# Optimization experiments

Hardware: AMD Instinct MI355X
Metric: run time of the kernel (lower is better)

The kernel has to match this reference:

```python
import jax, jax.numpy as jnp
import numpy as np

N_NODES = 50000
N_EDGES = 800000
NUM_RELATIONS = 8   # 2 * n_speakers**2 with n_speakers = 2
NUM_BASES = 30
G_DIM, H1_DIM, H2_DIM = 128, 128, 128


def setup_inputs() -> dict:
    key = jax.random.key(0)
    ks = jax.random.split(key, 10)
    inp = {
        "node_features": jax.random.normal(ks[0], (N_NODES, G_DIM), jnp.float32),
        "edge_index": jax.random.randint(ks[1], (2, N_EDGES), 0, N_NODES, dtype=jnp.int64),
        "edge_type": jax.random.randint(ks[2], (N_EDGES,), 0, NUM_RELATIONS, dtype=jnp.int64),
        "edge_norm": jax.random.uniform(ks[3], (N_EDGES,), jnp.float32),
        # RGCNConv params (basis decomposition)
        "basis": jax.random.normal(ks[4], (NUM_BASES, G_DIM, H1_DIM), jnp.float32) * 0.05,
        "comp": jax.random.normal(ks[5], (NUM_RELATIONS, NUM_BASES), jnp.float32) * 0.1,
        "root": jax.random.normal(ks[6], (G_DIM, H1_DIM), jnp.float32) * 0.05,
        "bias1": jnp.zeros((H1_DIM,), jnp.float32),
        # GraphConv params: lin_rel (with bias) applied to aggregated neighbors, lin_root (no bias)
        "w_rel": jax.random.normal(ks[7], (H1_DIM, H2_DIM), jnp.float32) * 0.05,
        "b_rel": jnp.zeros((H2_DIM,), jnp.float32),
        "w_root": jax.random.normal(ks[8], (H1_DIM, H2_DIM), jnp.float32) * 0.05,
    }
    return inp


def reference(node_features, edge_index, edge_type, edge_norm,
              basis, comp, root, bias1, w_rel, b_rel, w_root):
    src, dst = edge_index[0], edge_index[1]  # source_to_target flow (PyG default)

    # ---- Layer 1: RGCNConv with basis decomposition ----
    # W[r] = sum_b comp[r,b] * basis[b]  -> [R, g, h1]
    W = jnp.einsum('rb,bio->rio', comp, basis)
    # Project every node under every relation once (N*R*h1), then gather per edge.
    # Mathematically identical to per-edge x_j @ W[edge_type] but avoids an [E, g, h1] tensor.
    x_proj = jnp.einsum('ni,rio->nro', node_features, W)  # [N, R, h1]
    msg = x_proj[src, edge_type] * edge_norm[:, None]     # [E, h1]
    agg = jax.ops.segment_sum(msg, dst, num_segments=N_NODES)  # scatter-add to targets
    h = agg + node_features @ root + bias1                # [N, h1]

    # ---- Layer 2: GraphConv (aggr='add', no edge_weight) ----
    agg2 = jax.ops.segment_sum(h[src], dst, num_segments=N_NODES)  # [N, h1]
    out = agg2 @ w_rel + b_rel + h @ w_root               # [N, h2]
    return out
```

## Files before the change

kernel.cpp:

```cpp
#include <hip/hip_runtime.h>
#include <hip/hip_bf16.h>
#include <stdint.h>

#define N_NODES 50000
#define N_EDGES 800000
#define NREL    8
#define NBASES  30
#define DIM     128
#define NSLOT   9
#define NCAT    (NSLOT*DIM)
#define SCAN_NB ((N_NODES + 255) / 256)
#define NB_C    196
#define EPB_PLACE 2048
#define NBLK_PLACE ((N_EDGES + EPB_PLACE - 1) / EPB_PLACE)
#define M_T1    32
#define T1_BLOCKS ((N_NODES + M_T1 - 1) / M_T1)
#define APAD    1160
#define PREP_TOTAL  (NCAT * DIM + 2 * DIM * DIM)
#define PREP_BLKS   ((PREP_TOTAL + 255) / 256)
#define CONV_BLKS   ((N_NODES * DIM / 4 + 255) / 256)
#define HIST_BLKS   ((N_EDGES + 255) / 256)

typedef __attribute__((ext_vector_type(8))) short short8;
typedef __attribute__((ext_vector_type(4))) float floatx4;
typedef __hip_bfloat16  bf16;
typedef __hip_bfloat162 bf16x2;

__device__ inline ushort f2bu(float f) { bf16 b = __float2bfloat16(f); return *(ushort*)&b; }
__device__ inline float  bu2f(ushort u) { union { unsigned i; float f; } c; c.i = ((unsigned)u) << 16; return c.f; }

__global__ __launch_bounds__(256) void setup_kernel(const float* __restrict__ basis, const float* __restrict__ comp,
                                                    const float* __restrict__ root, const float* __restrict__ w_rel,
                                                    const float* __restrict__ w_root,
                                                    bf16* __restrict__ W2T, bf16* __restrict__ wrelT,
                                                    bf16* __restrict__ wrootT,
                                                    const float4* __restrict__ x4, ushort4* __restrict__ xb4,
                                                    const int* __restrict__ ei, int* __restrict__ deg) {
    int b = blockIdx.x;
    if (b < PREP_BLKS) {
        int idx = b * 256 + threadIdx.x;
        const int n_cat = NCAT * DIM;
        const int n_sq  = DIM * DIM;
        if (idx < n_cat) {
            int o = idx / NCAT;
            int rem = idx - o * NCAT;
            int r = rem >> 7, k = rem & 127;
            float v;
            if (r < NREL) {
                v = 0.f;
                for (int bb = 0; bb < NBASES; ++bb)
                    v += comp[r * NBASES + bb] * basis[(bb * DIM + k) * DIM + o];
            } else {
                v = root[k * DIM + o];
            }
            W2T[idx] = __float2bfloat16(v);
        } else if (idx < n_cat + n_sq) {
            int t = idx - n_cat; int k = t & 127, o = t >> 7;
            wrelT[o * DIM + k] = __float2bfloat16(w_rel[k * DIM + o]);
        } else if (idx < n_cat + 2 * n_sq) {
            int t = idx - n_cat - n_sq; int k = t & 127, o = t >> 7;
            wrootT[o * DIM + k] = __float2bfloat16(w_root[k * DIM + o]);
        }
    } else if (b < PREP_BLKS + CONV_BLKS) {
        int i = (b - PREP_BLKS) * 256 + threadIdx.x;
        int n4 = N_NODES * DIM / 4;
        if (i < n4) {
            float4 f = x4[i];
            ushort4 o;
            o.x = f2bu(f.x); o.y = f2bu(f.y); o.z = f2bu(f.z); o.w = f2bu(f.w);
            xb4[i] = o;
        }
    } else {
        int e = (b - PREP_BLKS - CONV_BLKS) * 256 + threadIdx.x;
        if (e < N_EDGES) atomicAdd(&deg[ei[N_EDGES + e]], 1);
    }
}

__global__ __launch_bounds__(256) void scan_one(const int* __restrict__ deg, int* __restrict__ segoff,
                                                unsigned long long* __restrict__ bstate, int n) {
    __shared__ int buf[256];
    int b = blockIdx.x, tid = threadIdx.x;
    int i = b * 256 + tid;
    int v = (i < n) ? deg[i] : 0;
    buf[tid] = v;
    __syncthreads();
#pragma unroll
    for (int o = 1; o < 256; o <<= 1) {
        int t = (tid >= o) ? buf[tid - o] : 0;
        __syncthreads();
        buf[tid] += t;
        __syncthreads();
    }
    int incl = buf[tid];
    int total = buf[255];
    if (tid == 0)
        __hip_atomic_store(&bstate[b], (1ULL << 32) | (unsigned)total,
                           __ATOMIC_RELEASE, __HIP_MEMORY_SCOPE_AGENT);
    int mysum = 0;
    for (int j = tid; j < b; j += 256) {
        unsigned long long s;
        do {
            s = __hip_atomic_load(&bstate[j], __ATOMIC_ACQUIRE, __HIP_MEMORY_SCOPE_AGENT);
        } while (!(s >> 32));
        mysum += (int)(s & 0xFFFFFFFFu);
    }
    __syncthreads();
    buf[tid] = mysum;
    __syncthreads();
#pragma unroll
    for (int o = 128; o > 0; o >>= 1) {
        if (tid < o) buf[tid] += buf[tid + o];
        __syncthreads();
    }
    int base = buf[0];
    if (i < n) segoff[i + 1] = base + incl;
    if (b == 0 && tid == 0) segoff[0] = 0;
}

__global__ __launch_bounds__(256) void place_kernel(const int* __restrict__ ei, const int* __restrict__ et,
                                                    const float* __restrict__ en, const int* __restrict__ segoff,
                                                    int* __restrict__ bcur, uint2* __restrict__ tmp) {
    __shared__ int lhist[NB_C];
    __shared__ int lbase[NB_C];
    __shared__ int lrank[NB_C];
    int tid = threadIdx.x;
    for (int i = tid; i < NB_C; i += 256) { lhist[i] = 0; lrank[i] = 0; }
    __syncthreads();
    int e0 = blockIdx.x * EPB_PLACE;
#pragma unroll
    for (int i = 0; i < EPB_PLACE / 256; ++i) {
        int e = e0 + i * 256 + tid;
        if (e < N_EDGES) atomicAdd(&lhist[ei[N_EDGES + e] >> 8], 1);
    }
    __syncthreads();
    for (int c = tid; c < NB_C; c += 256)
        if (lhist[c] > 0) lbase[c] = atomicAdd(&bcur[c], lhist[c]);
    __syncthreads();
#pragma unroll
    for (int i = 0; i < EPB_PLACE / 256; ++i) {
        int e = e0 + i * 256 + tid;
        if (e < N_EDGES) {
            int d = ei[N_EDGES + e];
            int c = d >> 8;
            int r = atomicAdd(&lrank[c], 1);
            int p = segoff[c << 8] + lbase[c] + r;
            tmp[p] = make_uint2((unsigned)ei[e] | ((unsigned)et[e] << 16) | ((unsigned)(d & 255) << 19),
                                __float_as_uint(en[e]));
        }
    }
}

__global__ __launch_bounds__(256) void sortb_kernel(const uint2* __restrict__ tmp, const int* __restrict__ segoff,
                                                    uint2* __restrict__ rec, int* __restrict__ typeoff) {
    __shared__ int hist2[256 * 8];
    int c = blockIdx.x;
    int tid = threadIdx.x;
    for (int i = tid; i < 256 * 8; i += 256) hist2[i] = 0;
    __syncthreads();
    int base = segoff[c << 8];
    int nlimit = (c + 1) << 8; if (nlimit > N_NODES) nlimit = N_NODES;
    int end = segoff[nlimit];
    for (int i = base + tid; i < end; i += 256) {
        unsigned x = tmp[i].x;
        int dl = (x >> 19) & 255, ty = (x >> 16) & 7;
        atomicAdd(&hist2[dl * 8 + ty], 1);
    }
    __syncthreads();
    {
        int node = (c << 8) + tid;
        if (node < N_NODES) {
            int run = segoff[node] - base;
            int offs[8];
#pragma unroll
            for (int t = 0; t < 8; ++t) {
                int cnt = hist2[tid * 8 + t];
                hist2[tid * 8 + t] = run;
                offs[t] = base + run;
                run += cnt;
            }
            *(int4*)(typeoff + (size_t)node * 8)     = make_int4(offs[0], offs[1], offs[2], offs[3]);
            *(int4*)(typeoff + (size_t)node * 8 + 4) = make_int4(offs[4], offs[5], offs[6], offs[7]);
        }
    }
    __syncthreads();
    for (int i = base + tid; i < end; i += 256) {
        uint2 r = tmp[i];
        int dl = (r.x >> 19) & 255, ty = (r.x >> 16) & 7;
        int p = base + atomicAdd(&hist2[dl * 8 + ty], 1);
        rec[p] = make_uint2(r.x & 0x7FFFFu, r.y);
    }
}

__device__ inline void flush8(ushort* dst, const float* acc) {
    short8 o;
#pragma unroll
    for (int f = 0; f < 8; ++f) o[f] = (short)f2bu(acc[f]);
    *(short8*)dst = o;
}

__global__ __launch_bounds__(512, 4) void rgcn1_kernel(const uint2* __restrict__ rec, const int* __restrict__ typeoff,
                                                       const int* __restrict__ segoff, const ushort* __restrict__ xb,
                                                       const ushort* __restrict__ W2Tu, const float* __restrict__ bias1,
                                                       ushort* __restrict__ H) {
    __shared__ ushort As[M_T1][APAD];
    int tm = blockIdx.x * M_T1;
    int tid = threadIdx.x;
    int quad = tid >> 4, kl = tid & 15;
    int node = tm + quad;

    int offs[10];
    if (node < N_NODES) {
        int4 o0 = *(const int4*)(typeoff + (size_t)node * 8);
        int4 o1 = *(const int4*)(typeoff + (size_t)node * 8 + 4);
        offs[0] = o0.x; offs[1] = o0.y; offs[2] = o0.z; offs[3] = o0.w;
        offs[4] = o1.x; offs[5] = o1.y; offs[6] = o1.z; offs[7] = o1.w;
        offs[8] = segoff[node + 1];
    } else {
#pragma unroll
        for (int t = 0; t < 9; ++t) offs[t] = 0;
    }
#pragma unroll
    for (int t = 0; t < 8; ++t) {
        float a8[8] = {0.f, 0.f, 0.f, 0.f, 0.f, 0.f, 0.f, 0.f};
        for (int eo = offs[t]; eo < offs[t + 1]; eo += 4) {
            int m = offs[t + 1] - eo; if (m > 4) m = 4;
            uint2 rr[4]; short8 vv[4];
#pragma unroll
            for (int j = 0; j < 4; ++j) if (j < m) rr[j] = rec[eo + j];
#pragma unroll
            for (int j = 0; j < 4; ++j) if (j < m)
                vv[j] = *(const short8*)(xb + (size_t)(rr[j].x & 0xFFFFu) * 128 + kl * 8);
#pragma unroll
            for (int j = 0; j < 4; ++j) if (j < m) {
                float nrm = __uint_as_float(rr[j].y);
#pragma unroll
                for (int f = 0; f < 8; ++f) a8[f] += nrm * bu2f((ushort)vv[j][f]);
            }
        }
        flush8(&As[quad][t * 128 + kl * 8], a8);
    }
    {
        short8 v = {0, 0, 0, 0, 0, 0, 0, 0};
        if (node < N_NODES) v = *(const short8*)(xb + (size_t)node * 128 + kl * 8);
        *(short8*)(&As[quad][8 * 128 + kl * 8]) = v;
    }
    __syncthreads();

    int wave = tid >> 6, lane = tid & 63;
    int q = lane >> 4, mr = lane & 15;
    floatx4 zero = {0.f, 0.f, 0.f, 0.f};
    floatx4 acc[2] = {zero, zero};
    const ushort* brow = W2Tu + (size_t)(wave * 16 + mr) * NCAT + q * 8;
    for (int kt = 0; kt < 36; ++kt) {
        short8 b  = *(const short8*)(brow + kt * 32);
        short8 a0 = *(const short8*)(&As[mr][kt * 32 + q * 8]);
        short8 a1 = *(const short8*)(&As[16 + mr][kt * 32 + q * 8]);
        acc[0] = __builtin_amdgcn_mfma_f32_16x16x32_bf16(a0, b, acc[0], 0, 0, 0);
        acc[1] = __builtin_amdgcn_mfma_f32_16x16x32_bf16(a1, b, acc[1], 0, 0, 0);
    }
    float bi = bias1[wave * 16 + mr];
#pragma unroll
    for (int rt = 0; rt < 2; ++rt)
#pragma unroll
        for (int r4 = 0; r4 < 4; ++r4) {
            int row = tm + rt * 16 + q * 4 + r4;
            if (row < N_NODES) H[(size_t)row * 128 + wave * 16 + mr] = f2bu(acc[rt][r4] + bi);
        }
}

__global__ void seg2_kernel(const uint2* __restrict__ rec, const int* __restrict__ segoff,
                            const ushort* __restrict__ h, ushort* __restrict__ out2) {
    int quad = threadIdx.x >> 4;
    int node = blockIdx.x * 16 + quad;
    if (node >= N_NODES) return;
    int lane = threadIdx.x & 15;
    int st = segoff[node], en = segoff[node + 1];
    float acc[8] = {0.f, 0.f, 0.f, 0.f, 0.f, 0.f, 0.f, 0.f};
    for (int chunk = st; chunk < en; chunk += 4) {
        int m = en - chunk; if (m > 4) m = 4;
        uint2 rr[4]; short8 vv[4];
#pragma unroll
        for (int j = 0; j < 4; ++j) if (j < m) rr[j] = rec[chunk + j];
#pragma unroll
        for (int j = 0; j < 4; ++j) if (j < m)
            vv[j] = *(const short8*)(h + (size_t)(rr[j].x & 0xFFFFu) * 128 + lane * 8);
#pragma unroll
        for (int j = 0; j < 4; ++j) if (j < m)
#pragma unroll
            for (int f = 0; f < 8; ++f) acc[f] += bu2f((ushort)vv[j][f]);
    }
    short8 o;
#pragma unroll
    for (int f = 0; f < 8; ++f) o[f] = (short)f2bu(acc[f]);
    *(short8*)(out2 + (size_t)node * 128 + lane * 8) = o;
}

__global__ __launch_bounds__(256) void gemm2_kernel(const bf16* __restrict__ A1, const bf16* __restrict__ B1T,
                                                    const bf16* __restrict__ A2, const bf16* __restrict__ B2T,
                                                    const float* __restrict__ brel, float* __restrict__ out, int M) {
    __shared__ ushort As[64][136];
    __shared__ ushort Bs[64][136];
    int tm = blockIdx.x * 64, tn = blockIdx.y * 64;
    int wave = threadIdx.x >> 6, lane = threadIdx.x & 63;
    int q = lane >> 4, mr = lane & 15;
    floatx4 zero = {0.f, 0.f, 0.f, 0.f};
    floatx4 acc[4] = {zero, zero, zero, zero};

    for (int phase = 0; phase < 2; ++phase) {
        const ushort* Au = (const ushort*)(phase ? A2 : A1);
        const ushort* Bu = (const ushort*)(phase ? B2T : B1T);
        if (phase) __syncthreads();
        for (int c = threadIdx.x; c < 64 * 16; c += 256) {
            int row = c >> 4, seg = c & 15;
            int gr = tm + row;
            short8 av = {0, 0, 0, 0, 0, 0, 0, 0};
            if (gr < M) av = *(const short8*)(Au + (size_t)gr * 128 + seg * 8);
            *(short8*)(&As[row][seg * 8]) = av;
            short8 bv = *(const short8*)(Bu + (size_t)(tn + row) * 128 + seg * 8);
            *(short8*)(&Bs[row][seg * 8]) = bv;
        }
        __syncthreads();
#pragma unroll
        for (int kt = 0; kt < 4; ++kt) {
            short8 a = *(const short8*)(&As[wave * 16 + mr][q * 8 + kt * 32]);
#pragma unroll
            for (int nt = 0; nt < 4; ++nt) {
                short8 b = *(const short8*)(&Bs[nt * 16 + mr][q * 8 + kt * 32]);
                acc[nt] = __builtin_amdgcn_mfma_f32_16x16x32_bf16(a, b, acc[nt], 0, 0, 0);
            }
        }
    }
    __syncthreads();
    float* Csf = (float*)&As[0][0];
#pragma unroll
    for (int nt = 0; nt < 4; ++nt)
#pragma unroll
        for (int r4 = 0; r4 < 4; ++r4) {
            int row = wave * 16 + q * 4 + r4;
            int col = nt * 16 + mr;
            Csf[row * 68 + col] = acc[nt][r4] + brel[tn + col];
        }
    __syncthreads();
#pragma unroll
    for (int u = 0; u < 4; ++u) {
        int cc = threadIdx.x + u * 256;
        int row = cc >> 4, seg = cc & 15;
        int gr = tm + row;
        if (gr < M) {
            float4 v = *(const float4*)(&Csf[row * 68 + seg * 4]);
            *(float4*)(out + (size_t)gr * 128 + tn + seg * 4) = v;
        }
    }
}

extern "C" void kernel_launch(void* const* d_in, const int* in_sizes, int n_in,
                              void* d_out, int out_size, void* d_ws, size_t ws_size,
                              hipStream_t stream) {
    const float* x      = (const float*)d_in[0];
    const int*   ei     = (const int*)d_in[1];
    const int*   et     = (const int*)d_in[2];
    const float* en     = (const float*)d_in[3];
    const float* basis  = (const float*)d_in[4];
    const float* comp   = (const float*)d_in[5];
    const float* root   = (const float*)d_in[6];
    const float* bias1  = (const float*)d_in[7];
    const float* w_rel  = (const float*)d_in[8];
    const float* b_rel  = (const float*)d_in[9];
    const float* w_root = (const float*)d_in[10];
    float* out = (float*)d_out;

    char* ws = (char*)d_ws;
    size_t off = 0;
    auto alloc = [&](size_t bytes) { size_t o = off; off += (bytes + 255) & ~(size_t)255; return o; };

    size_t o_deg    = alloc((size_t)N_NODES * 4);
    size_t o_bcur   = alloc((size_t)NB_C * 4);
    size_t o_bstate = alloc((size_t)SCAN_NB * 8);
    size_t o_segoff = alloc((size_t)(N_NODES + 1) * 4);
    size_t o_toff   = alloc((size_t)N_NODES * 8 * 4);
    size_t o_rec    = alloc((size_t)N_EDGES * 8);
    size_t o_tmp    = alloc((size_t)N_EDGES * 8);
    size_t o_w2t    = alloc((size_t)NCAT * DIM * 2);
    size_t o_wrel   = alloc((size_t)DIM * DIM * 2);
    size_t o_wroot  = alloc((size_t)DIM * DIM * 2);
    size_t o_xb     = alloc((size_t)N_NODES * DIM * 2);
    size_t o_hb     = alloc((size_t)N_NODES * DIM * 2);
    size_t o_agg2   = alloc((size_t)N_NODES * DIM * 2);

    int*   deg    = (int*)(ws + o_deg);
    int*   bcur   = (int*)(ws + o_bcur);
    unsigned long long* bstate = (unsigned long long*)(ws + o_bstate);
    int*   segoff = (int*)(ws + o_segoff);
    int*   toff   = (int*)(ws + o_toff);
    uint2* rec    = (uint2*)(ws + o_rec);
    uint2* tmp    = (uint2*)(ws + o_tmp);
    bf16*  w2t    = (bf16*)(ws + o_w2t);
    bf16*  wrelT  = (bf16*)(ws + o_wrel);
    bf16*  wrootT = (bf16*)(ws + o_wroot);
    bf16*  xb     = (bf16*)(ws + o_xb);
    bf16*  hb     = (bf16*)(ws + o_hb);
    bf16*  agg2   = (bf16*)(ws + o_agg2);

    hipMemsetAsync(ws + o_deg, 0, o_segoff - o_deg, stream);

    setup_kernel<<<PREP_BLKS + CONV_BLKS + HIST_BLKS, 256, 0, stream>>>(
        basis, comp, root, w_rel, w_root, w2t, wrelT, wrootT,
        (const float4*)x, (ushort4*)xb, ei, deg);
    scan_one<<<SCAN_NB, 256, 0, stream>>>(deg, segoff, bstate, N_NODES);
    place_kernel<<<NBLK_PLACE, 256, 0, stream>>>(ei, et, en, segoff, bcur, tmp);
    sortb_kernel<<<NB_C, 256, 0, stream>>>(tmp, segoff, rec, toff);
    rgcn1_kernel<<<T1_BLOCKS, 512, 0, stream>>>(rec, toff, segoff, (const ushort*)xb,
                                                (const ushort*)w2t, bias1, (ushort*)hb);
    seg2_kernel<<<(N_NODES + 15) / 16, 256, 0, stream>>>(rec, segoff, (const ushort*)hb, (ushort*)agg2);
    {
        dim3 grid((N_NODES + 63) / 64, DIM / 64);
        gemm2_kernel<<<grid, 256, 0, stream>>>(agg2, wrelT, hb, wrootT, b_rel, out, N_NODES);
    }
}
```

Measured before the change: 367.7 us.

## Halve rgcn1 node tile to 16 and deepen edge gather batches to 8

The RGCN layer-1 kernel now handles 16 nodes per block with 256 threads instead of 32 nodes with 512. Each wave computes two 16-column output tiles, so one LDS A-fragment is reused against two B-fragments. Bounds checks are removed because 50000 divides evenly by 16. Both gather loops in rgcn1 and seg2 now batch 8 edges instead of 4 to keep more loads in flight. This costs more registers, and each block re-reads the full bf16 weight matrix from global/L2 for half as many rows, doubling weight traffic.

```diff
diff --git a/kernel.cpp b/kernel.cpp
--- a/kernel.cpp
+++ b/kernel.cpp
@@ -13,7 +13,7 @@
 #define NB_C    196
 #define EPB_PLACE 2048
 #define NBLK_PLACE ((N_EDGES + EPB_PLACE - 1) / EPB_PLACE)
-#define M_T1    32
+#define M_T1    16
 #define T1_BLOCKS ((N_NODES + M_T1 - 1) / M_T1)
 #define APAD    1160
 #define PREP_TOTAL  (NCAT * DIM + 2 * DIM * DIM)
@@ -198,7 +198,7 @@
     *(short8*)dst = o;
 }
 
-__global__ __launch_bounds__(512, 4) void rgcn1_kernel(const uint2* __restrict__ rec, const int* __restrict__ typeoff,
+__global__ __launch_bounds__(256, 4) void rgcn1_kernel(const uint2* __restrict__ rec, const int* __restrict__ typeoff,
                                                        const int* __restrict__ segoff, const ushort* __restrict__ xb,
                                                        const ushort* __restrict__ W2Tu, const float* __restrict__ bias1,
                                                        ushort* __restrict__ H) {
@@ -209,29 +209,26 @@
     int node = tm + quad;
 
     int offs[10];
-    if (node < N_NODES) {
+    {
         int4 o0 = *(const int4*)(typeoff + (size_t)node * 8);
         int4 o1 = *(const int4*)(typeoff + (size_t)node * 8 + 4);
         offs[0] = o0.x; offs[1] = o0.y; offs[2] = o0.z; offs[3] = o0.w;
         offs[4] = o1.x; offs[5] = o1.y; offs[6] = o1.z; offs[7] = o1.w;
         offs[8] = segoff[node + 1];
-    } else {
-#pragma unroll
-        for (int t = 0; t < 9; ++t) offs[t] = 0;
     }
 #pragma unroll
     for (int t = 0; t < 8; ++t) {
         float a8[8] = {0.f, 0.f, 0.f, 0.f, 0.f, 0.f, 0.f, 0.f};
-        for (int eo = offs[t]; eo < offs[t + 1]; eo += 4) {
-            int m = offs[t + 1] - eo; if (m > 4) m = 4;
-            uint2 rr[4]; short8 vv[4];
-#pragma unroll
-            for (int j = 0; j < 4; ++j) if (j < m) rr[j] = rec[eo + j];
-#pragma unroll
-            for (int j = 0; j < 4; ++j) if (j < m)
+        for (int eo = offs[t]; eo < offs[t + 1]; eo += 8) {
+            int m = offs[t + 1] - eo; if (m > 8) m = 8;
+            uint2 rr[8]; short8 vv[8];
+#pragma unroll
+            for (int j = 0; j < 8; ++j) if (j < m) rr[j] = rec[eo + j];
+#pragma unroll
+            for (int j = 0; j < 8; ++j) if (j < m)
                 vv[j] = *(const short8*)(xb + (size_t)(rr[j].x & 0xFFFFu) * 128 + kl * 8);
 #pragma unroll
-            for (int j = 0; j < 4; ++j) if (j < m) {
+            for (int j = 0; j < 8; ++j) if (j < m) {
                 float nrm = __uint_as_float(rr[j].y);
 #pragma unroll
                 for (int f = 0; f < 8; ++f) a8[f] += nrm * bu2f((ushort)vv[j][f]);
@@ -239,33 +236,30 @@
         }
         flush8(&As[quad][t * 128 + kl * 8], a8);
     }
-    {
-        short8 v = {0, 0, 0, 0, 0, 0, 0, 0};
-        if (node < N_NODES) v = *(const short8*)(xb + (size_t)node * 128 + kl * 8);
-        *(short8*)(&As[quad][8 * 128 + kl * 8]) = v;
-    }
+    *(short8*)(&As[quad][8 * 128 + kl * 8]) = *(const short8*)(xb + (size_t)node * 128 + kl * 8);
     __syncthreads();
 
     int wave = tid >> 6, lane = tid & 63;
     int q = lane >> 4, mr = lane & 15;
     floatx4 zero = {0.f, 0.f, 0.f, 0.f};
-    floatx4 acc[2] = {zero, zero};
-    const ushort* brow = W2Tu + (size_t)(wave * 16 + mr) * NCAT + q * 8;
+    floatx4 acc0 = zero, acc1 = zero;
+    const ushort* b0row = W2Tu + (size_t)(wave * 32 + mr) * NCAT + q * 8;
+    const ushort* b1row = W2Tu + (size_t)(wave * 32 + 16 + mr) * NCAT + q * 8;
     for (int kt = 0; kt < 36; ++kt) {
-        short8 b  = *(const short8*)(brow + kt * 32);
-        short8 a0 = *(const short8*)(&As[mr][kt * 32 + q * 8]);
-        short8 a1 = *(const short8*)(&As[16 + mr][kt * 32 + q * 8]);
-        acc[0] = __builtin_amdgcn_mfma_f32_16x16x32_bf16(a0, b, acc[0], 0, 0, 0);
-        acc[1] = __builtin_amdgcn_mfma_f32_16x16x32_bf16(a1, b, acc[1], 0, 0, 0);
-    }
-    float bi = bias1[wave * 16 + mr];
-#pragma unroll
-    for (int rt = 0; rt < 2; ++rt)
-#pragma unroll
-        for (int r4 = 0; r4 < 4; ++r4) {
-            int row = tm + rt * 16 + q * 4 + r4;
-            if (row < N_NODES) H[(size_t)row * 128 + wave * 16 + mr] = f2bu(acc[rt][r4] + bi);
-        }
+        short8 a  = *(const short8*)(&As[mr][kt * 32 + q * 8]);
+        short8 b0 = *(const short8*)(b0row + kt * 32);
+        short8 b1 = *(const short8*)(b1row + kt * 32);
+        acc0 = __builtin_amdgcn_mfma_f32_16x16x32_bf16(a, b0, acc0, 0, 0, 0);
+        acc1 = __builtin_amdgcn_mfma_f32_16x16x32_bf16(a, b1, acc1, 0, 0, 0);
+    }
+    float bi0 = bias1[wave * 32 + mr];
+    float bi1 = bias1[wave * 32 + 16 + mr];
+#pragma unroll
+    for (int r4 = 0; r4 < 4; ++r4) {
+        int row = tm + q * 4 + r4;
+        H[(size_t)row * 128 + wave * 32 + mr]      = f2bu(acc0[r4] + bi0);
+        H[(size_t)row * 128 + wave * 32 + 16 + mr] = f2bu(acc1[r4] + bi1);
+    }
 }
 
 __global__ void seg2_kernel(const uint2* __restrict__ rec, const int* __restrict__ segoff,
@@ -276,16 +270,16 @@
     int lane = threadIdx.x & 15;
     int st = segoff[node], en = segoff[node + 1];
     float acc[8] = {0.f, 0.f, 0.f, 0.f, 0.f, 0.f, 0.f, 0.f};
-    for (int chunk = st; chunk < en; chunk += 4) {
-        int m = en - chunk; if (m > 4) m = 4;
-        uint2 rr[4]; short8 vv[4];
-#pragma unroll
-        for (int j = 0; j < 4; ++j) if (j < m) rr[j] = rec[chunk + j];
-#pragma unroll
-        for (int j = 0; j < 4; ++j) if (j < m)
+    for (int chunk = st; chunk < en; chunk += 8) {
+        int m = en - chunk; if (m > 8) m = 8;
+        uint2 rr[8]; short8 vv[8];
+#pragma unroll
+        for (int j = 0; j < 8; ++j) if (j < m) rr[j] = rec[chunk + j];
+#pragma unroll
+        for (int j = 0; j < 8; ++j) if (j < m)
             vv[j] = *(const short8*)(h + (size_t)(rr[j].x & 0xFFFFu) * 128 + lane * 8);
 #pragma unroll
-        for (int j = 0; j < 4; ++j) if (j < m)
+        for (int j = 0; j < 8; ++j) if (j < m)
 #pragma unroll
             for (int f = 0; f < 8; ++f) acc[f] += bu2f((ushort)vv[j][f]);
     }
@@ -409,7 +403,7 @@
     scan_one<<<SCAN_NB, 256, 0, stream>>>(deg, segoff, bstate, N_NODES);
     place_kernel<<<NBLK_PLACE, 256, 0, stream>>>(ei, et, en, segoff, bcur, tmp);
     sortb_kernel<<<NB_C, 256, 0, stream>>>(tmp, segoff, rec, toff);
-    rgcn1_kernel<<<T1_BLOCKS, 512, 0, stream>>>(rec, toff, segoff, (const ushort*)xb,
+    rgcn1_kernel<<<T1_BLOCKS, 256, 0, stream>>>(rec, toff, segoff, (const ushort*)xb,
                                                 (const ushort*)w2t, bias1, (ushort*)hb);
     seg2_kernel<<<(N_NODES + 15) / 16, 256, 0, stream>>>(rec, segoff, (const ushort*)hb, (ushort*)agg2);
     {
```

Measured after the change: 402.7 us. 9.5% more time.
